# Performance work log

Measured on AMD Instinct MI355X. Metric: run time of the kernel, lower is better.

The kernel has to match this reference:

```python
import jax, jax.numpy as jnp
import numpy as np

NUM_CAMS = 1
NUM_HEADS = 1
NUM_LEVELS = 1
NUM_POINTS = 4
NUM_DEPTH = 128
EMBED = 128  # must equal NUM_DEPTH (output_proj is applied to the depth axis)


def setup_inputs() -> dict:
    key0 = jax.random.key(0)
    ks = jax.random.split(key0, 12)
    bsv, nq, nv = 1, 1024, 1024  # nq == nv == H*W (32*32)
    off_dim = NUM_CAMS * NUM_HEADS * NUM_LEVELS * NUM_DEPTH * NUM_POINTS * 2  # 1024
    aw_dim = NUM_CAMS * NUM_HEADS * NUM_LEVELS * NUM_DEPTH * NUM_POINTS       # 512
    return {
        "query": jax.random.normal(ks[0], (bsv, nq, EMBED), jnp.float32),
        "key": jax.random.normal(ks[1], (NUM_CAMS, nv, bsv, EMBED), jnp.float32),
        "value": jax.random.normal(ks[2], (NUM_CAMS, nv, bsv, EMBED), jnp.float32),
        "ref_3d": jax.random.uniform(ks[3], (bsv * NUM_CAMS, nq * NUM_DEPTH, 2), jnp.float32),
        "spatial_shapes": jnp.array([[32, 32]], dtype=jnp.int32),
        "W_off": jax.random.normal(ks[4], (EMBED, off_dim), jnp.float32) * 0.02,
        "b_off": jax.random.normal(ks[5], (off_dim,), jnp.float32) * 0.02,
        "W_attn": jax.random.normal(ks[6], (EMBED, aw_dim), jnp.float32) * 0.02,
        "b_attn": jax.random.normal(ks[7], (aw_dim,), jnp.float32) * 0.02,
        "W_v": jax.random.normal(ks[8], (EMBED, EMBED), jnp.float32) / np.sqrt(EMBED),
        "b_v": jnp.zeros((EMBED,), jnp.float32),
        "W_o": jax.random.normal(ks[9], (EMBED, EMBED), jnp.float32) / np.sqrt(EMBED),
        "b_o": jnp.zeros((EMBED,), jnp.float32),
    }


def _bilinear_sample(val, H, W, x, y):
    """grid_sample(align_corners=False, padding=zeros) equivalent.
    val: [B, H*W, D]; x, y: [B, Q, P] in pixel coords. Returns [B, Q, P, D]."""
    B, Q, P = x.shape
    D = val.shape[-1]
    x0f = jnp.floor(x); y0f = jnp.floor(y)
    ix0 = x0f.astype(jnp.int32); iy0 = y0f.astype(jnp.int32)
    wx1 = x - x0f; wy1 = y - y0f
    wx0 = 1.0 - wx1; wy0 = 1.0 - wy1

    def corner(ix, iy, w):
        valid = (ix >= 0) & (ix < W) & (iy >= 0) & (iy < H)
        idx = jnp.clip(iy, 0, H - 1) * W + jnp.clip(ix, 0, W - 1)  # [B,Q,P]
        g = jnp.take_along_axis(val, idx.reshape(B, Q * P)[:, :, None], axis=1)
        g = g.reshape(B, Q, P, D)
        return g * (w * valid.astype(val.dtype))[..., None]

    return (corner(ix0, iy0, wx0 * wy0)
            + corner(ix0 + 1, iy0, wx1 * wy0)
            + corner(ix0, iy0 + 1, wx0 * wy1)
            + corner(ix0 + 1, iy0 + 1, wx1 * wy1))


def reference(query, key, value, ref_3d, spatial_shapes,
              W_off, b_off, W_attn, b_attn, W_v, b_v, W_o, b_o):
    bsv, nq, E = query.shape
    cams, nv, bs, _ = key.shape
    identity = query

    # key/value: [cams, nv, bs, E] -> [bsv, nv, E]
    key2 = jnp.transpose(key, (2, 0, 1, 3)).reshape(bsv, nv, E)
    val = jnp.flip(value, axis=0)
    val = jnp.transpose(val, (2, 0, 1, 3)).reshape(bsv, nv, E)
    val = val @ W_v + b_v
    val = val.reshape(bsv * cams, nv, E)  # num_heads=1 -> head_dim=E

    # offsets / attention weights (heads=levels=1 axes squeezed)
    off = (query @ W_off + b_off).reshape(bsv, nq, cams, NUM_DEPTH, NUM_POINTS, 2)
    aw = (query @ W_attn + b_attn).reshape(bsv, nq, cams, NUM_DEPTH, NUM_LEVELS * NUM_POINTS)
    aw = jax.nn.softmax(aw, axis=-1).reshape(bsv, nq, cams, NUM_DEPTH, NUM_POINTS)
    off = jnp.transpose(off, (0, 2, 1, 3, 4, 5)).reshape(bsv * cams, nq * NUM_DEPTH, NUM_POINTS, 2)
    aw = jnp.transpose(aw, (0, 2, 1, 3, 4)).reshape(bsv * cams, nq * NUM_DEPTH, NUM_POINTS)

    H = spatial_shapes[0, 0]
    W = spatial_shapes[0, 1]
    norm = jnp.stack([W, H]).astype(off.dtype)  # [W, H]
    loc = ref_3d[:, :, None, :] + off / norm    # [B, Qe, P, 2] in [0,1]
    x = loc[..., 0] * W.astype(loc.dtype) - 0.5
    y = loc[..., 1] * H.astype(loc.dtype) - 0.5

    sampled = _bilinear_sample(val, H, W, x, y)          # [B, Qe, P, E]
    out = jnp.einsum('bqpe,bqp->bqe', sampled, aw)       # weighted sum over points

    out = out.reshape(bsv, cams, nq, NUM_DEPTH, E).mean(axis=1)  # [bsv, nq, depth, E]
    out = (out * key2[:, :, None, :]).mean(axis=-1)              # [bsv, nq, depth]
    out = out @ W_o + b_o                                        # depth == EMBED
    return out + identity  # dropout = identity in eval
```

## Files before the change

### kernel.cpp

```cpp
#include <hip/hip_runtime.h>


#define NQ   1024
#define NV   1024
#define ND   128
#define NP   4
#define IMG_W 32
#define IMG_H 32

typedef __attribute__((ext_vector_type(8))) short bfx8;
typedef __attribute__((ext_vector_type(4))) float f32x4;

__device__ __forceinline__ unsigned short bf_rne(float f) {
  unsigned u = __float_as_uint(f);
  return (unsigned short)((u + 0x7FFFu + ((u >> 16) & 1u)) >> 16);
}

__device__ __forceinline__ void gemm_tile64(
    const float* __restrict__ A, const float* __restrict__ B,
    int N, bool nt,
    const float* __restrict__ bias, const float* __restrict__ cvec,
    float* __restrict__ C, int m0, int n0, float* sA, float* sB) {
  const int tid = threadIdx.x;
#pragma unroll
  for (int k = 0; k < 8; ++k) {
    int c = tid + k * 256;
    int m = c & 63, e4 = c >> 6;
    const float4 v = *(const float4*)(A + (size_t)(m0 + m) * 128 + e4 * 4);
    sA[(e4 * 4 + 0) * 64 + m] = v.x;
    sA[(e4 * 4 + 1) * 64 + m] = v.y;
    sA[(e4 * 4 + 2) * 64 + m] = v.z;
    sA[(e4 * 4 + 3) * 64 + m] = v.w;
  }
  if (nt) {
#pragma unroll
    for (int k = 0; k < 8; ++k) {
      int c = tid + k * 256;
      int n = c & 63, e4 = c >> 6;
      const float4 v = *(const float4*)(B + (size_t)(n0 + n) * 128 + e4 * 4);
      sB[(e4 * 4 + 0) * 64 + n] = v.x;
      sB[(e4 * 4 + 1) * 64 + n] = v.y;
      sB[(e4 * 4 + 2) * 64 + n] = v.z;
      sB[(e4 * 4 + 3) * 64 + n] = v.w;
    }
  } else {
#pragma unroll
    for (int k = 0; k < 8; ++k) {
      int c = tid + k * 256;
      int n4 = c & 15, e = c >> 4;
      *(float4*)(sB + e * 64 + n4 * 4) =
          *(const float4*)(B + (size_t)e * N + n0 + n4 * 4);
    }
  }
  __syncthreads();

  const int tx = tid & 15, ty = tid >> 4;
  float acc[4][4] = {};
#pragma unroll 8
  for (int e = 0; e < 128; ++e) {
    const float4 a = *(const float4*)(sA + e * 64 + ty * 4);
    const float4 b = *(const float4*)(sB + e * 64 + tx * 4);
    acc[0][0] += a.x * b.x; acc[0][1] += a.x * b.y; acc[0][2] += a.x * b.z; acc[0][3] += a.x * b.w;
    acc[1][0] += a.y * b.x; acc[1][1] += a.y * b.y; acc[1][2] += a.y * b.z; acc[1][3] += a.y * b.w;
    acc[2][0] += a.z * b.x; acc[2][1] += a.z * b.y; acc[2][2] += a.z * b.z; acc[2][3] += a.z * b.w;
    acc[3][0] += a.w * b.x; acc[3][1] += a.w * b.y; acc[3][2] += a.w * b.z; acc[3][3] += a.w * b.w;
  }

  float4 bv = make_float4(0.f, 0.f, 0.f, 0.f);
  if (bias) bv = *(const float4*)(bias + n0 + tx * 4);
#pragma unroll
  for (int i = 0; i < 4; ++i) {
    const int m = m0 + ty * 4 + i;
    float cv = cvec ? cvec[m] : 0.f;
    float4 r;
    r.x = acc[i][0] + bv.x + cv;
    r.y = acc[i][1] + bv.y + cv;
    r.z = acc[i][2] + bv.z + cv;
    r.w = acc[i][3] + bv.w + cv;
    *(float4*)(C + (size_t)m * 128 + n0 + tx * 4) = r;
  }
}

__device__ __forceinline__ void transpose64(const float* __restrict__ src, int N,
                                            int n0, float* __restrict__ dst,
                                            float* lds) {
  const int tid = threadIdx.x;
#pragma unroll
  for (int it = 0; it < 8; ++it) {
    int c = tid + it * 256;
    int k = c >> 4, cf = c & 15;
    float4 v = *(const float4*)(src + (size_t)k * N + n0 + cf * 4);
    lds[k * 65 + cf * 4 + 0] = v.x;
    lds[k * 65 + cf * 4 + 1] = v.y;
    lds[k * 65 + cf * 4 + 2] = v.z;
    lds[k * 65 + cf * 4 + 3] = v.w;
  }
  __syncthreads();
#pragma unroll
  for (int it = 0; it < 8; ++it) {
    int c = tid + it * 256;
    int dn = c >> 5, kq = c & 31;
    float4 v;
    v.x = lds[(kq * 4 + 0) * 65 + dn];
    v.y = lds[(kq * 4 + 1) * 65 + dn];
    v.z = lds[(kq * 4 + 2) * 65 + dn];
    v.w = lds[(kq * 4 + 3) * 65 + dn];
    *(float4*)(dst + (size_t)(n0 + dn) * 128 + kq * 4) = v;
  }
}

__global__ __launch_bounds__(256, 2) void d1_kernel(
    const float* __restrict__ key, const float* __restrict__ W_v,
    const float* __restrict__ b_v, const float* __restrict__ W_off,
    const float* __restrict__ W_attn,
    float* __restrict__ keyp_ws, float* __restrict__ c_ws,
    float* __restrict__ wofft, float* __restrict__ wattnt) {
  __shared__ float smem[16384];
  const int t = blockIdx.x;
  if (t < 16) {
    transpose64(W_off, 1024, t * 64, wofft, smem);
  } else if (t < 24) {
    transpose64(W_attn, 512, (t - 16) * 64, wattnt, smem);
  } else if (t < 56) {
    const int u = t - 24;
    gemm_tile64(key, W_v, 128, true, nullptr, nullptr, keyp_ws,
                (u >> 1) * 64, (u & 1) * 64, smem, smem + 8192);
  } else {
    for (int i = 0; i < 4; ++i) {
      const int q = threadIdx.x + i * 256;
      float s = 0.f;
      for (int e = 0; e < 128; ++e) s += key[(size_t)q * 128 + e] * b_v[e];
      c_ws[q] = s;
    }
  }
}

__device__ __forceinline__ void mfma_tile128(
    const float* __restrict__ A,
    const float* __restrict__ B,
    const float* __restrict__ bias,
    const float* __restrict__ cvec,
    float* __restrict__ C, int ldc,
    int m0, int n0, unsigned short* sA, unsigned short* sB) {
  const int tid = threadIdx.x;

  {
    const float* srcs[2] = {A, B};
    const int r0s[2] = {m0, n0};
    unsigned short* dsts[2] = {sA, sB};
#pragma unroll
    for (int s = 0; s < 2; ++s) {
      const float* src = srcs[s];
      const int r0 = r0s[s];
      unsigned short* dst = dsts[s];
#pragma unroll
      for (int it = 0; it < 8; ++it) {
        int c = tid + it * 256;
        int r = c >> 4, cc = c & 15;
        const float* p = src + (size_t)(r0 + r) * 128 + cc * 8;
        float4 f0 = *(const float4*)p;
        float4 f1 = *(const float4*)(p + 4);
        bfx8 v;
        v[0] = (short)bf_rne(f0.x); v[1] = (short)bf_rne(f0.y);
        v[2] = (short)bf_rne(f0.z); v[3] = (short)bf_rne(f0.w);
        v[4] = (short)bf_rne(f1.x); v[5] = (short)bf_rne(f1.y);
        v[6] = (short)bf_rne(f1.z); v[7] = (short)bf_rne(f1.w);
        int byte = r * 256 + ((cc * 16) ^ ((r & 15) << 4));
        *(bfx8*)((char*)dst + byte) = v;
      }
    }
  }
  __syncthreads();

  const int l = tid & 63;
  const int w = tid >> 6;
  const int wr = w >> 1, wc = w & 1;
  const int lr = l & 15, g = l >> 4;

  f32x4 acc[4][4];
#pragma unroll
  for (int mi = 0; mi < 4; ++mi)
#pragma unroll
    for (int ni = 0; ni < 4; ++ni) {
      f32x4 z = {0.f, 0.f, 0.f, 0.f};
      acc[mi][ni] = z;
    }

#pragma unroll
  for (int ks = 0; ks < 4; ++ks) {
    const int colb = (ks * 64 + g * 16) ^ (lr << 4);
    bfx8 af[4], bfr[4];
#pragma unroll
    for (int mi = 0; mi < 4; ++mi) {
      int r = wr * 64 + mi * 16 + lr;
      af[mi] = *(const bfx8*)((const char*)sA + r * 256 + colb);
    }
#pragma unroll
    for (int ni = 0; ni < 4; ++ni) {
      int r = wc * 64 + ni * 16 + lr;
      bfr[ni] = *(const bfx8*)((const char*)sB + r * 256 + colb);
    }
#pragma unroll
    for (int mi = 0; mi < 4; ++mi)
#pragma unroll
      for (int ni = 0; ni < 4; ++ni)
        acc[mi][ni] = __builtin_amdgcn_mfma_f32_16x16x32_bf16(
            af[mi], bfr[ni], acc[mi][ni], 0, 0, 0);
  }

#pragma unroll
  for (int mi = 0; mi < 4; ++mi) {
    float cv[4];
#pragma unroll
    for (int i = 0; i < 4; ++i) {
      int row = m0 + wr * 64 + mi * 16 + g * 4 + i;
      cv[i] = cvec ? cvec[row] : 0.f;
    }
#pragma unroll
    for (int ni = 0; ni < 4; ++ni) {
      int col = n0 + wc * 64 + ni * 16 + lr;
      float bn = bias ? bias[col] : 0.f;
#pragma unroll
      for (int i = 0; i < 4; ++i) {
        int row = m0 + wr * 64 + mi * 16 + g * 4 + i;
        C[(size_t)row * ldc + col] = acc[mi][ni][i] + bn + cv[i];
      }
    }
  }
}

__global__ __launch_bounds__(256, 2) void d2_kernel(
    const float* __restrict__ query, const float* __restrict__ keyp,
    const float* __restrict__ value,
    const float* __restrict__ wofft, const float* __restrict__ wattnt,
    const float* __restrict__ b_off, const float* __restrict__ b_attn,
    const float* __restrict__ c_ws,
    float* __restrict__ off_ws, float* __restrict__ aw_ws,
    float* __restrict__ dotv_ws) {
  __shared__ __align__(16) unsigned short sAB[32768];
  unsigned short* sA = sAB;
  unsigned short* sB = sAB + 16384;
  const int t = blockIdx.x;
  if (t < 64) {
    mfma_tile128(query, wofft, b_off, nullptr, off_ws, 1024,
                 (t >> 3) * 128, (t & 7) * 128, sA, sB);
  } else if (t < 96) {
    const int u = t - 64;
    mfma_tile128(query, wattnt, b_attn, nullptr, aw_ws, 512,
                 (u >> 2) * 128, (u & 3) * 128, sA, sB);
  } else {
    const int u = t - 96;
    mfma_tile128(keyp, value, nullptr, c_ws, dotv_ws, 1024,
                 (u >> 3) * 128, (u & 7) * 128, sA, sB);
  }
}

__global__ __launch_bounds__(256) void p3_kernel(
    const float* __restrict__ dotv, const float* __restrict__ off,
    const float* __restrict__ awr, const float* __restrict__ ref3d,
    const float* __restrict__ query, const float* __restrict__ W_o,
    const float* __restrict__ b_o, float* __restrict__ out) {
  __shared__ float img[2][NV];
  __shared__ float o1s[2][ND];

  const int tid = threadIdx.x;
  const int q0 = blockIdx.x * 2;

#pragma unroll
  for (int k = 0; k < 2; ++k) {
    int c = tid + k * 256;
    int qq = c >> 8, v4 = c & 255;
    *(float4*)(&img[qq][v4 * 4]) =
        *(const float4*)(dotv + (size_t)(q0 + qq) * NV + v4 * 4);
  }
  __syncthreads();

  {
    const int qq = tid >> 7;
    const int q = q0 + qq;
    const int d = tid & 127;
    const float* im = img[qq];
    const size_t qe = (size_t)q * ND + d;

    const float rx = ref3d[qe * 2 + 0];
    const float ry = ref3d[qe * 2 + 1];

    const float* awp = awr + (size_t)q * (ND * NP) + d * NP;
    const float a0 = awp[0], a1 = awp[1], a2 = awp[2], a3 = awp[3];
    const float mx = fmaxf(fmaxf(a0, a1), fmaxf(a2, a3));
    const float e0 = __expf(a0 - mx), e1 = __expf(a1 - mx),
                e2 = __expf(a2 - mx), e3 = __expf(a3 - mx);
    const float inv = 1.0f / (e0 + e1 + e2 + e3);
    const float wgt4[4] = {e0 * inv, e1 * inv, e2 * inv, e3 * inv};

    const float* op = off + (size_t)q * (ND * NP * 2) + d * (NP * 2);

    float acc = 0.0f;
#pragma unroll
    for (int p = 0; p < NP; ++p) {
      const float x = rx * (float)IMG_W + op[p * 2 + 0] - 0.5f;
      const float y = ry * (float)IMG_H + op[p * 2 + 1] - 0.5f;
      const float xf = floorf(x), yf = floorf(y);
      const int ix0 = (int)xf, iy0 = (int)yf;
      const float wx1 = x - xf, wy1 = y - yf;
      const float wx0 = 1.0f - wx1, wy0 = 1.0f - wy1;

      float s = 0.0f;
#pragma unroll
      for (int cy = 0; cy < 2; ++cy) {
#pragma unroll
        for (int cx = 0; cx < 2; ++cx) {
          const int ix = ix0 + cx, iy = iy0 + cy;
          const bool valid = (ix >= 0) & (ix < IMG_W) & (iy >= 0) & (iy < IMG_H);
          const int cix = min(max(ix, 0), IMG_W - 1);
          const int ciy = min(max(iy, 0), IMG_H - 1);
          const float wgt = (cx ? wx1 : wx0) * (cy ? wy1 : wy0);
          s += valid ? im[ciy * IMG_W + cix] * wgt : 0.0f;
        }
      }
      acc += wgt4[p] * s;
    }
    o1s[qq][d] = acc * (1.0f / 128.0f);
  }
  __syncthreads();

  {
    const int qq = tid >> 7;
    const int q = q0 + qq;
    const int n = tid & 127;
    float acc = b_o[n] + query[(size_t)q * 128 + n];
#pragma unroll 8
    for (int d = 0; d < 128; ++d)
      acc += o1s[qq][d] * W_o[(size_t)d * 128 + n];
    out[(size_t)q * 128 + n] = acc;
  }
}

extern "C" void kernel_launch(void* const* d_in, const int* in_sizes, int n_in,
                              void* d_out, int out_size, void* d_ws, size_t ws_size,
                              hipStream_t stream) {
  const float* query  = (const float*)d_in[0];
  const float* key    = (const float*)d_in[1];
  const float* value  = (const float*)d_in[2];
  const float* ref3d  = (const float*)d_in[3];
  const float* W_off  = (const float*)d_in[5];
  const float* b_off  = (const float*)d_in[6];
  const float* W_attn = (const float*)d_in[7];
  const float* b_attn = (const float*)d_in[8];
  const float* W_v    = (const float*)d_in[9];
  const float* b_v    = (const float*)d_in[10];
  const float* W_o    = (const float*)d_in[11];
  const float* b_o    = (const float*)d_in[12];
  float* out = (float*)d_out;

  float* ws = (float*)d_ws;
  float* off_ws  = ws;
  float* aw_ws   = off_ws + (size_t)NQ * 1024;
  float* keyp_ws = aw_ws + (size_t)NQ * 512;
  float* c_ws    = keyp_ws + (size_t)NQ * 128;
  float* dotv_ws = c_ws + 1024;
  float* wofft   = dotv_ws + (size_t)NQ * 1024;
  float* wattnt  = wofft + (size_t)1024 * 128;

  d1_kernel<<<57, 256, 0, stream>>>(key, W_v, b_v, W_off, W_attn,
                                    keyp_ws, c_ws, wofft, wattnt);
  d2_kernel<<<160, 256, 0, stream>>>(query, keyp_ws, value, wofft, wattnt,
                                     b_off, b_attn, c_ws,
                                     off_ws, aw_ws, dotv_ws);
  p3_kernel<<<512, 256, 0, stream>>>(dotv_ws, off_ws, aw_ws, ref3d, query,
                                     W_o, b_o, out);
}
```

Before: 111.0 us.

## Fuse three kernels into one cooperative kernel with grid-wide syncs

Merges the preprocessing, GEMM and sampling/output kernels into a single cooperative launch of 512 blocks, separating the stages with threadfence plus grid.sync. This removes two kernel launch boundaries and their gaps. In exchange the first two stages leave most blocks idle at the barriers, and with 64KB static shared memory and 2 blocks per CU, all 512 blocks must be co-resident for the cooperative launch to succeed.

New measurement: 346.3 us. 3.12x slower.

```diff
diff --git a/kernel.cpp b/kernel.cpp
--- a/kernel.cpp
+++ b/kernel.cpp
@@ -1,4 +1,7 @@
 #include <hip/hip_runtime.h>
+#include <hip/hip_cooperative_groups.h>
+
+namespace cg = cooperative_groups;
 
 
 #define NQ   1024
@@ -106,32 +109,6 @@
     v.z = lds[(kq * 4 + 2) * 65 + dn];
     v.w = lds[(kq * 4 + 3) * 65 + dn];
     *(float4*)(dst + (size_t)(n0 + dn) * 128 + kq * 4) = v;
-  }
-}
-
-__global__ __launch_bounds__(256, 2) void d1_kernel(
-    const float* __restrict__ key, const float* __restrict__ W_v,
-    const float* __restrict__ b_v, const float* __restrict__ W_off,
-    const float* __restrict__ W_attn,
-    float* __restrict__ keyp_ws, float* __restrict__ c_ws,
-    float* __restrict__ wofft, float* __restrict__ wattnt) {
-  __shared__ float smem[16384];
-  const int t = blockIdx.x;
-  if (t < 16) {
-    transpose64(W_off, 1024, t * 64, wofft, smem);
-  } else if (t < 24) {
-    transpose64(W_attn, 512, (t - 16) * 64, wattnt, smem);
-  } else if (t < 56) {
-    const int u = t - 24;
-    gemm_tile64(key, W_v, 128, true, nullptr, nullptr, keyp_ws,
-                (u >> 1) * 64, (u & 1) * 64, smem, smem + 8192);
-  } else {
-    for (int i = 0; i < 4; ++i) {
-      const int q = threadIdx.x + i * 256;
-      float s = 0.f;
-      for (int e = 0; e < 128; ++e) s += key[(size_t)q * 128 + e] * b_v[e];
-      c_ws[q] = s;
-    }
   }
 }
 
@@ -229,110 +206,136 @@
   }
 }
 
-__global__ __launch_bounds__(256, 2) void d2_kernel(
-    const float* __restrict__ query, const float* __restrict__ keyp,
-    const float* __restrict__ value,
-    const float* __restrict__ wofft, const float* __restrict__ wattnt,
-    const float* __restrict__ b_off, const float* __restrict__ b_attn,
-    const float* __restrict__ c_ws,
+__global__ __launch_bounds__(256, 2) void fused_kernel(
+    const float* __restrict__ query, const float* __restrict__ key,
+    const float* __restrict__ value, const float* __restrict__ ref3d,
+    const float* __restrict__ W_off, const float* __restrict__ b_off,
+    const float* __restrict__ W_attn, const float* __restrict__ b_attn,
+    const float* __restrict__ W_v, const float* __restrict__ b_v,
+    const float* __restrict__ W_o, const float* __restrict__ b_o,
     float* __restrict__ off_ws, float* __restrict__ aw_ws,
-    float* __restrict__ dotv_ws) {
-  __shared__ __align__(16) unsigned short sAB[32768];
-  unsigned short* sA = sAB;
-  unsigned short* sB = sAB + 16384;
-  const int t = blockIdx.x;
-  if (t < 64) {
-    mfma_tile128(query, wofft, b_off, nullptr, off_ws, 1024,
-                 (t >> 3) * 128, (t & 7) * 128, sA, sB);
-  } else if (t < 96) {
-    const int u = t - 64;
-    mfma_tile128(query, wattnt, b_attn, nullptr, aw_ws, 512,
-                 (u >> 2) * 128, (u & 3) * 128, sA, sB);
-  } else {
-    const int u = t - 96;
-    mfma_tile128(keyp, value, nullptr, c_ws, dotv_ws, 1024,
-                 (u >> 3) * 128, (u & 7) * 128, sA, sB);
-  }
-}
-
-__global__ __launch_bounds__(256) void p3_kernel(
-    const float* __restrict__ dotv, const float* __restrict__ off,
-    const float* __restrict__ awr, const float* __restrict__ ref3d,
-    const float* __restrict__ query, const float* __restrict__ W_o,
-    const float* __restrict__ b_o, float* __restrict__ out) {
-  __shared__ float img[2][NV];
-  __shared__ float o1s[2][ND];
-
+    float* __restrict__ keyp_ws, float* __restrict__ c_ws,
+    float* __restrict__ dotv_ws, float* __restrict__ wofft,
+    float* __restrict__ wattnt, float* __restrict__ out) {
+  __shared__ __align__(16) char smem[65536];
+  cg::grid_group grid = cg::this_grid();
+  const int b = blockIdx.x;
   const int tid = threadIdx.x;
-  const int q0 = blockIdx.x * 2;
-
-#pragma unroll
-  for (int k = 0; k < 2; ++k) {
-    int c = tid + k * 256;
-    int qq = c >> 8, v4 = c & 255;
-    *(float4*)(&img[qq][v4 * 4]) =
-        *(const float4*)(dotv + (size_t)(q0 + qq) * NV + v4 * 4);
-  }
-  __syncthreads();
+
+  if (b < 16) {
+    transpose64(W_off, 1024, b * 64, wofft, (float*)smem);
+  } else if (b < 24) {
+    transpose64(W_attn, 512, (b - 16) * 64, wattnt, (float*)smem);
+  } else if (b < 56) {
+    const int u = b - 24;
+    gemm_tile64(key, W_v, 128, true, nullptr, nullptr, keyp_ws,
+                (u >> 1) * 64, (u & 1) * 64, (float*)smem,
+                (float*)smem + 8192);
+  } else if (b == 56) {
+    for (int i = 0; i < 4; ++i) {
+      const int q = tid + i * 256;
+      float s = 0.f;
+      for (int e = 0; e < 128; ++e) s += key[(size_t)q * 128 + e] * b_v[e];
+      c_ws[q] = s;
+    }
+  }
+
+  __threadfence();
+  grid.sync();
 
   {
-    const int qq = tid >> 7;
-    const int q = q0 + qq;
-    const int d = tid & 127;
-    const float* im = img[qq];
-    const size_t qe = (size_t)q * ND + d;
-
-    const float rx = ref3d[qe * 2 + 0];
-    const float ry = ref3d[qe * 2 + 1];
-
-    const float* awp = awr + (size_t)q * (ND * NP) + d * NP;
-    const float a0 = awp[0], a1 = awp[1], a2 = awp[2], a3 = awp[3];
-    const float mx = fmaxf(fmaxf(a0, a1), fmaxf(a2, a3));
-    const float e0 = __expf(a0 - mx), e1 = __expf(a1 - mx),
-                e2 = __expf(a2 - mx), e3 = __expf(a3 - mx);
-    const float inv = 1.0f / (e0 + e1 + e2 + e3);
-    const float wgt4[4] = {e0 * inv, e1 * inv, e2 * inv, e3 * inv};
-
-    const float* op = off + (size_t)q * (ND * NP * 2) + d * (NP * 2);
-
-    float acc = 0.0f;
-#pragma unroll
-    for (int p = 0; p < NP; ++p) {
-      const float x = rx * (float)IMG_W + op[p * 2 + 0] - 0.5f;
-      const float y = ry * (float)IMG_H + op[p * 2 + 1] - 0.5f;
-      const float xf = floorf(x), yf = floorf(y);
-      const int ix0 = (int)xf, iy0 = (int)yf;
-      const float wx1 = x - xf, wy1 = y - yf;
-      const float wx0 = 1.0f - wx1, wy0 = 1.0f - wy1;
-
-      float s = 0.0f;
-#pragma unroll
-      for (int cy = 0; cy < 2; ++cy) {
-#pragma unroll
-        for (int cx = 0; cx < 2; ++cx) {
-          const int ix = ix0 + cx, iy = iy0 + cy;
-          const bool valid = (ix >= 0) & (ix < IMG_W) & (iy >= 0) & (iy < IMG_H);
-          const int cix = min(max(ix, 0), IMG_W - 1);
-          const int ciy = min(max(iy, 0), IMG_H - 1);
-          const float wgt = (cx ? wx1 : wx0) * (cy ? wy1 : wy0);
-          s += valid ? im[ciy * IMG_W + cix] * wgt : 0.0f;
+    unsigned short* sA = (unsigned short*)smem;
+    unsigned short* sB = sA + 16384;
+    if (b < 64) {
+      mfma_tile128(query, wofft, b_off, nullptr, off_ws, 1024,
+                   (b >> 3) * 128, (b & 7) * 128, sA, sB);
+    } else if (b < 96) {
+      const int u = b - 64;
+      mfma_tile128(query, wattnt, b_attn, nullptr, aw_ws, 512,
+                   (u >> 2) * 128, (u & 3) * 128, sA, sB);
+    } else if (b < 160) {
+      const int u = b - 96;
+      mfma_tile128(keyp_ws, value, nullptr, c_ws, dotv_ws, 1024,
+                   (u >> 3) * 128, (u & 7) * 128, sA, sB);
+    }
+  }
+
+  __threadfence();
+  grid.sync();
+
+  {
+    float* img = (float*)smem;
+    float* o1s = (float*)smem + 2048;
+    const int q0 = b * 2;
+
+#pragma unroll
+    for (int k = 0; k < 2; ++k) {
+      int c = tid + k * 256;
+      int qq = c >> 8, v4 = c & 255;
+      *(float4*)(&img[qq * NV + v4 * 4]) =
+          *(const float4*)(dotv_ws + (size_t)(q0 + qq) * NV + v4 * 4);
+    }
+    __syncthreads();
+
+    {
+      const int qq = tid >> 7;
+      const int q = q0 + qq;
+      const int d = tid & 127;
+      const float* im = img + qq * NV;
+      const size_t qe = (size_t)q * ND + d;
+
+      const float rx = ref3d[qe * 2 + 0];
+      const float ry = ref3d[qe * 2 + 1];
+
+      const float* awp = aw_ws + (size_t)q * (ND * NP) + d * NP;
+      const float a0 = awp[0], a1 = awp[1], a2 = awp[2], a3 = awp[3];
+      const float mx = fmaxf(fmaxf(a0, a1), fmaxf(a2, a3));
+      const float e0 = __expf(a0 - mx), e1 = __expf(a1 - mx),
+                  e2 = __expf(a2 - mx), e3 = __expf(a3 - mx);
+      const float inv = 1.0f / (e0 + e1 + e2 + e3);
+      const float wgt4[4] = {e0 * inv, e1 * inv, e2 * inv, e3 * inv};
+
+      const float* op = off_ws + (size_t)q * (ND * NP * 2) + d * (NP * 2);
+
+      float acc = 0.0f;
+#pragma unroll
+      for (int p = 0; p < NP; ++p) {
+        const float x = rx * (float)IMG_W + op[p * 2 + 0] - 0.5f;
+        const float y = ry * (float)IMG_H + op[p * 2 + 1] - 0.5f;
+        const float xf = floorf(x), yf = floorf(y);
+        const int ix0 = (int)xf, iy0 = (int)yf;
+        const float wx1 = x - xf, wy1 = y - yf;
+        const float wx0 = 1.0f - wx1, wy0 = 1.0f - wy1;
+
+        float s = 0.0f;
+#pragma unroll
+        for (int cy = 0; cy < 2; ++cy) {
+#pragma unroll
+          for (int cx = 0; cx < 2; ++cx) {
+            const int ix = ix0 + cx, iy = iy0 + cy;
+            const bool valid = (ix >= 0) & (ix < IMG_W) & (iy >= 0) & (iy < IMG_H);
+            const int cix = min(max(ix, 0), IMG_W - 1);
+            const int ciy = min(max(iy, 0), IMG_H - 1);
+            const float wgt = (cx ? wx1 : wx0) * (cy ? wy1 : wy0);
+            s += valid ? im[ciy * IMG_W + cix] * wgt : 0.0f;
+          }
         }
+        acc += wgt4[p] * s;
       }
-      acc += wgt4[p] * s;
-    }
-    o1s[qq][d] = acc * (1.0f / 128.0f);
-  }
-  __syncthreads();
-
-  {
-    const int qq = tid >> 7;
-    const int q = q0 + qq;
-    const int n = tid & 127;
-    float acc = b_o[n] + query[(size_t)q * 128 + n];
+      o1s[qq * ND + d] = acc * (1.0f / 128.0f);
+    }
+    __syncthreads();
+
+    {
+      const int qq = tid >> 7;
+      const int q = q0 + qq;
+      const int n = tid & 127;
+      float acc = b_o[n] + query[(size_t)q * 128 + n];
 #pragma unroll 8
-    for (int d = 0; d < 128; ++d)
-      acc += o1s[qq][d] * W_o[(size_t)d * 128 + n];
-    out[(size_t)q * 128 + n] = acc;
+      for (int d = 0; d < 128; ++d)
+        acc += o1s[qq * ND + d] * W_o[(size_t)d * 128 + n];
+      out[(size_t)q * 128 + n] = acc;
+    }
   }
 }
 
@@ -362,11 +365,13 @@
   float* wofft   = dotv_ws + (size_t)NQ * 1024;
   float* wattnt  = wofft + (size_t)1024 * 128;
 
-  d1_kernel<<<57, 256, 0, stream>>>(key, W_v, b_v, W_off, W_attn,
-                                    keyp_ws, c_ws, wofft, wattnt);
-  d2_kernel<<<160, 256, 0, stream>>>(query, keyp_ws, value, wofft, wattnt,
-                                     b_off, b_attn, c_ws,
-                                     off_ws, aw_ws, dotv_ws);
-  p3_kernel<<<512, 256, 0, stream>>>(dotv_ws, off_ws, aw_ws, ref3d, query,
-                                     W_o, b_o, out);
-}
+  void* args[] = {
+      (void*)&query, (void*)&key, (void*)&value, (void*)&ref3d,
+      (void*)&W_off, (void*)&b_off, (void*)&W_attn, (void*)&b_attn,
+      (void*)&W_v, (void*)&b_v, (void*)&W_o, (void*)&b_o,
+      (void*)&off_ws, (void*)&aw_ws, (void*)&keyp_ws, (void*)&c_ws,
+      (void*)&dotv_ws, (void*)&wofft, (void*)&wattnt, (void*)&out};
+
+  hipLaunchCooperativeKernel((const void*)fused_kernel, dim3(512), dim3(256),
+                             args, 0, stream);
+}
```
